# Performance work log

Measured on AMD Instinct MI355X. Metric: run time of the kernel, lower is better.

The kernel has to match this reference:

```python
import jax, jax.numpy as jnp
import numpy as np

B, N, J = 8, 2048, 1024
QD, CD, H, D = 1024, 768, 16, 64
INNER = H * D


def setup_inputs() -> dict:
    key = jax.random.key(0)
    ks = jax.random.split(key, 7)
    s = 0.02
    return {
        "x": jax.random.normal(ks[0], (B, N, QD), jnp.float32),
        "context": jax.random.normal(ks[1], (B, J, CD), jnp.float32),
        "Wq": jax.random.normal(ks[2], (QD, INNER), jnp.float32) * s,
        "Wk": jax.random.normal(ks[3], (CD, INNER), jnp.float32) * s,
        "Wv": jax.random.normal(ks[4], (CD, INNER), jnp.float32) * s,
        "Wo": jax.random.normal(ks[5], (INNER, QD), jnp.float32) * s,
        "bo": jnp.zeros((QD,), jnp.float32),
    }


def reference(x, context, Wq, Wk, Wv, Wo, bo):
    scale = D ** (-0.5)
    # projections, then split heads: b n (h d) -> b h n d
    q = (x @ Wq).reshape(B, N, H, D).transpose(0, 2, 1, 3)
    k = (context @ Wk).reshape(B, J, H, D).transpose(0, 2, 1, 3)
    v = (context @ Wv).reshape(B, J, H, D).transpose(0, 2, 1, 3)
    sim = jnp.einsum("bhid,bhjd->bhij", q, k) * scale  # [B,H,N,J]
    attn = jax.nn.softmax(sim, axis=-1)
    out = jnp.einsum("bhij,bhjd->bhid", attn, v)  # [B,H,N,D]
    out = out.transpose(0, 2, 1, 3).reshape(B, N, INNER)
    return out @ Wo + bo
```

## Files before the change

kernel.cpp:

```cpp
#include <hip/hip_runtime.h>

#define B_     8
#define N_     2048
#define J_     1024
#define QD_    1024
#define CD_    768
#define H_     16
#define D_     64
#define INNER_ 1024

typedef __attribute__((ext_vector_type(8)))  __bf16 bf16x8;
typedef __attribute__((ext_vector_type(4)))  __bf16 bf16x4;
typedef __attribute__((ext_vector_type(4)))  float  f32x4;
typedef __attribute__((ext_vector_type(16))) float  f32x16;
typedef __attribute__((ext_vector_type(2)))  unsigned uint2v;

__device__ __forceinline__ __bf16 to_bf16(float f) { return (__bf16)f; }

__device__ __forceinline__ unsigned pack2(float lo, float hi) {
    union { __bf16 h; unsigned short u; } a, b;
    a.h = (__bf16)lo; b.h = (__bf16)hi;
    return (unsigned)a.u | ((unsigned)b.u << 16);
}

__global__ __launch_bounds__(256)
void cvt_all(const float* __restrict__ x, const float* __restrict__ ctx,
             __bf16* __restrict__ xb, __bf16* __restrict__ cb)
{
    const int nx = (B_ * N_ * QD_) / 4;
    const int nc = (B_ * J_ * CD_) / 4;
    int i = blockIdx.x * 256 + threadIdx.x;
    if (i < nx) {
        float4 v = ((const float4*)x)[i];
        bf16x4 o;
        o[0] = (__bf16)v.x; o[1] = (__bf16)v.y; o[2] = (__bf16)v.z; o[3] = (__bf16)v.w;
        ((bf16x4*)xb)[i] = o;
    } else if (i < nx + nc) {
        float4 v = ((const float4*)ctx)[i - nx];
        bf16x4 o;
        o[0] = (__bf16)v.x; o[1] = (__bf16)v.y; o[2] = (__bf16)v.z; o[3] = (__bf16)v.w;
        ((bf16x4*)cb)[i - nx] = o;
    }
}

__global__ __launch_bounds__(256)
void transpose_all(const float* __restrict__ Wq, const float* __restrict__ Wk,
                   const float* __restrict__ Wv, const float* __restrict__ Wo,
                   __bf16* __restrict__ wqt, __bf16* __restrict__ wkt,
                   __bf16* __restrict__ wvt, __bf16* __restrict__ wot, float sq)
{
    __shared__ float tile[32][33];
    const int z = blockIdx.z;
    const float* W;  __bf16* Wt;  int K;  float scale = 1.f;
    if (z == 0)      { W = Wq; Wt = wqt; K = QD_;   scale = sq; }
    else if (z == 1) { W = Wk; Wt = wkt; K = CD_; }
    else if (z == 2) { W = Wv; Wt = wvt; K = CD_; }
    else             { W = Wo; Wt = wot; K = INNER_; }
    const int N = 1024;
    const int n0 = blockIdx.x * 32;
    const int k0 = blockIdx.y * 32;
    if (k0 >= K) return;
    const int tx = threadIdx.x & 31;
    const int ty = threadIdx.x >> 5;
#pragma unroll
    for (int r = 0; r < 32; r += 8)
        tile[ty + r][tx] = W[(size_t)(k0 + ty + r) * N + n0 + tx];
    __syncthreads();
#pragma unroll
    for (int r = 0; r < 32; r += 8)
        Wt[(size_t)(n0 + ty + r) * K + k0 + tx] = to_bf16(tile[tx][ty + r] * scale);
}

template<int FINAL, int KDIM>
__device__ __forceinline__
void core8(const __bf16* __restrict__ A, const __bf16* __restrict__ Bt,
           __bf16* __restrict__ Cb, __bf16* __restrict__ Cb2, float* __restrict__ Cf,
           const float* __restrict__ bias, int N, int work,
           __bf16 (&sA)[2][16384], __bf16 (&sB)[2][16384])
{
    constexpr int NIT = KDIM / 64;

    const int tid = threadIdx.x;
    const int wid = tid >> 6;
    const int l   = tid & 63;
    const int lo  = l & 15, hi = (l >> 4) & 3;

    const int gn = N >> 8;
    const int m0 = (work / gn) * 256;
    const int n0 = (work % gn) * 256;

    const int wm  = (wid >> 2) * 128, wn = (wid & 3) * 64;
    const int wmr = (wid >> 2) * 8,   bnr = (wid & 3) * 4;

    int rOff[2], cOff[2], dOff[2];
#pragma unroll
    for (int n = 0; n < 2; ++n) {
        const int s = n * 8 + wid;
        rOff[n] = (s >> 1) * 16 + (l >> 2);
        cOff[n] = (s & 1) * 32 + (((l & 3) * 8) ^ (((l >> 5) & 1) * 16));
        dOff[n] = n * 4096 + wid * 512;
    }

    const int inner = lo * 32 + ((hi * 8) ^ ((lo >> 3) * 16));

    f32x4 acc[8][4] = {};
    bf16x8 af[4][2], bfr[4][2];

#define STAGE8(nb, h, kt) do { \
    _Pragma("unroll") \
    for (int n = 0; n < 2; ++n) { \
        const __bf16* gp = ((h) < 2 ? A + (size_t)(m0 + ((h) & 1) * 128 + rOff[n]) * KDIM \
                                    : Bt + (size_t)(n0 + ((h) & 1) * 128 + rOff[n]) * KDIM) \
                           + (kt) + cOff[n]; \
        __bf16* dp = ((h) < 2 ? &sA[nb][((h) & 1) * 8192 + dOff[n]] \
                              : &sB[nb][((h) & 1) * 8192 + dOff[n]]); \
        __builtin_amdgcn_global_load_lds((const __attribute__((address_space(1))) void*)gp, \
                                         (__attribute__((address_space(3))) void*)dp, 16, 0, 0); \
    } } while (0)

#define RD_A(x0, cnt, nb) do { \
    _Pragma("unroll") \
    for (int x = 0; x < (cnt); ++x) \
        _Pragma("unroll") \
        for (int kk = 0; kk < 2; ++kk) \
            af[x][kk] = *(const bf16x8*)&sA[nb][((wmr + (x0) + x) * 2 + kk) * 512 + inner]; \
    } while (0)

#define RD_B(j0, cnt, nb) do { \
    _Pragma("unroll") \
    for (int j = 0; j < (cnt); ++j) \
        _Pragma("unroll") \
        for (int kk = 0; kk < 2; ++kk) \
            bfr[(j0) + j][kk] = *(const bf16x8*)&sB[nb][((bnr + (j0) + j) * 2 + kk) * 512 + inner]; \
    } while (0)

#define MMQ(mh, nh) do { \
    __builtin_amdgcn_s_setprio(1); \
    _Pragma("unroll") \
    for (int x = 0; x < 4; ++x) \
        _Pragma("unroll") \
        for (int j = 0; j < 2; ++j) \
            _Pragma("unroll") \
            for (int kk = 0; kk < 2; ++kk) \
                acc[(mh) * 4 + x][(nh) * 2 + j] = __builtin_amdgcn_mfma_f32_16x16x32_bf16( \
                    af[x][kk], bfr[(nh) * 2 + j][kk], acc[(mh) * 4 + x][(nh) * 2 + j], 0, 0, 0); \
    __builtin_amdgcn_s_setprio(0); \
    } while (0)

#define BARR() do { __builtin_amdgcn_s_barrier(); \
    asm volatile("" ::: "memory"); __builtin_amdgcn_sched_barrier(0); } while (0)

#pragma unroll
    for (int h = 0; h < 4; ++h) STAGE8(0, h, 0);

    for (int it = 0; it < NIT; ++it) {
        const int nb = it & 1, nbn = nb ^ 1;
        const int ktn = (it + 1) * 64;
        const bool notlast = (it < NIT - 1);

        if (notlast) STAGE8(nbn, 0, ktn);
        if (notlast) asm volatile("s_waitcnt vmcnt(2)" ::: "memory");
        else         asm volatile("s_waitcnt vmcnt(0)" ::: "memory");
        BARR();
        RD_A(0, 4, nb); RD_B(0, 2, nb);
        MMQ(0, 0);
        BARR();
        if (notlast) STAGE8(nbn, 1, ktn);
        BARR();
        RD_B(2, 2, nb);
        MMQ(0, 1);
        BARR();
        if (notlast) STAGE8(nbn, 2, ktn);
        BARR();
        RD_A(4, 4, nb);
        MMQ(1, 0);
        BARR();
        if (notlast) STAGE8(nbn, 3, ktn);
        BARR();
        MMQ(1, 1);
        BARR();
    }
#undef STAGE8
#undef RD_A
#undef RD_B
#undef MMQ
#undef BARR

#pragma unroll
    for (int i = 0; i < 8; ++i) {
        const int row = m0 + wm + i * 16 + hi * 4;
#pragma unroll
        for (int j = 0; j < 4; ++j) {
            const int col = n0 + wn + j * 16 + lo;
            if (FINAL == 3) {
                if (col < 1024) {
#pragma unroll
                    for (int r = 0; r < 4; ++r)
                        Cb[(size_t)(row + r) * 1024 + col] = to_bf16(acc[i][j][r]);
                } else {
                    const int c2 = col - 1024;
                    const int head = c2 >> 6, d = c2 & 63;
                    const int bb = row >> 10, jj = row & 1023;
                    bf16x4 v4;
#pragma unroll
                    for (int r = 0; r < 4; ++r) v4[r] = to_bf16(acc[i][j][r]);
                    *(bf16x4*)&Cb2[(((size_t)(bb * 16 + head)) * 64 + d) * (size_t)J_ + jj] = v4;
                }
            } else {
#pragma unroll
                for (int r = 0; r < 4; ++r) {
                    if (FINAL == 1) Cf[(size_t)(row + r) * N + col] = acc[i][j][r] + bias[col];
                    else            Cb[(size_t)(row + r) * N + col] = to_bf16(acc[i][j][r]);
                }
            }
        }
    }
}

__global__ __launch_bounds__(512, 2)
void gemm_qkv(const __bf16* __restrict__ xb, const __bf16* __restrict__ wqt, __bf16* __restrict__ Qb,
              const __bf16* __restrict__ cb, const __bf16* __restrict__ wkt,
              __bf16* __restrict__ Kb, __bf16* __restrict__ Vt)
{
    __shared__ __bf16 sA[2][16384];
    __shared__ __bf16 sB[2][16384];
    const int blk = blockIdx.x;
    if (blk < 256) {
        const int work = (blk & 7) * 32 + (blk >> 3);
        core8<0, QD_>(xb, wqt, Qb, nullptr, nullptr, nullptr, INNER_, work, sA, sB);
    } else {
        const int hb = blk - 256;
        const int work = (hb & 7) * 32 + (hb >> 3);
        core8<3, CD_>(cb, wkt, Kb, Vt, nullptr, nullptr, 2 * INNER_, work, sA, sB);
    }
}

__global__ __launch_bounds__(512, 2)
void gemm_o(const __bf16* __restrict__ Ob, const __bf16* __restrict__ wot,
            float* __restrict__ out, const float* __restrict__ bias)
{
    __shared__ __bf16 sA[2][16384];
    __shared__ __bf16 sB[2][16384];
    const int blk = blockIdx.x;
    const int work = (blk & 7) * 32 + (blk >> 3);
    core8<1, INNER_>(Ob, wot, nullptr, nullptr, out, bias, QD_, work, sA, sB);
}

#define SEGE 544

__global__ __launch_bounds__(256, 4)
void attn2(const __bf16* __restrict__ Qb, const __bf16* __restrict__ Kb,
           const __bf16* __restrict__ Vt, __bf16* __restrict__ Ob)
{
    __shared__ __bf16 sK[2][8 * SEGE];
    __shared__ __bf16 sV[2][8 * SEGE];

    const int tid = threadIdx.x;
    const int wid = tid >> 6;
    const int l   = tid & 63;
    const int lq  = l & 31;
    const int hi  = l >> 5;

    const int blk  = blockIdx.x;
    const int work = (blk & 7) * 256 + (blk >> 3);
    const int qt = work & 15;
    const int h  = (work >> 4) & 15;
    const int b  = work >> 8;
    const int bh = b * H_ + h;

    bf16x8 qf[4];
    {
        const __bf16* qp = Qb + ((size_t)b * N_ + qt * 128 + wid * 32 + lq) * INNER_ + h * D_;
#pragma unroll
        for (int kc = 0; kc < 4; ++kc)
            qf[kc] = *(const bf16x8*)(qp + kc * 16 + hi * 8);
    }

    f32x16 accO[2] = {};
    float lsum = 0.f;

    const int srow = l >> 3, schk = l & 7;
    const __bf16* ksrc = Kb + ((size_t)b * J_ + wid * 8 + srow) * INNER_ + h * D_ + ((schk ^ srow) * 8);
    const __bf16* vsrc = Vt + ((size_t)bh * D_ + wid * 8 + srow) * J_ + ((schk ^ srow) * 8);

#define STAGE_T(bb, t) do { \
    _Pragma("unroll") \
    for (int c = 0; c < 2; ++c) { \
        __builtin_amdgcn_global_load_lds((const __attribute__((address_space(1))) void*)(ksrc + ((size_t)(t) * 64 + c * 32) * INNER_), \
            (__attribute__((address_space(3))) void*)(&sK[bb][(c * 4 + wid) * SEGE]), 16, 0, 0); \
        __builtin_amdgcn_global_load_lds((const __attribute__((address_space(1))) void*)(vsrc + (size_t)(c) * 32 * J_ + (t) * 64), \
            (__attribute__((address_space(3))) void*)(&sV[bb][(c * 4 + wid) * SEGE]), 16, 0, 0); \
    } } while (0)

    STAGE_T(0, 0);
    __syncthreads();

    for (int t = 0; t < J_ / 64; ++t) {
        const int bb = t & 1;
        if (t < J_ / 64 - 1) STAGE_T(bb ^ 1, t + 1);

        const __bf16* Ks = sK[bb];
        const __bf16* Vs = sV[bb];

#pragma unroll
        for (int jsub = 0; jsub < 2; ++jsub) {
            bf16x8 kf[4], vf[2][2];
            const int ksg = (jsub * 4 + (lq >> 3)) * SEGE + (lq & 7) * 64;
#pragma unroll
            for (int kc = 0; kc < 4; ++kc)
                kf[kc] = *(const bf16x8*)&Ks[ksg + (((kc * 2 + hi) ^ (lq & 7)) * 8)];
#pragma unroll
            for (int dt = 0; dt < 2; ++dt) {
                const int vsg = (dt * 4 + (lq >> 3)) * SEGE + (lq & 7) * 64;
#pragma unroll
                for (int k2 = 0; k2 < 2; ++k2)
                    vf[dt][k2] = *(const bf16x8*)&Vs[vsg + ((((jsub * 2 + k2) * 2 + hi) ^ (lq & 7)) * 8)];
            }

            f32x16 s = {};
            __builtin_amdgcn_s_setprio(1);
#pragma unroll
            for (int kc = 0; kc < 4; ++kc)
                s = __builtin_amdgcn_mfma_f32_32x32x16_bf16(kf[kc], qf[kc], s, 0, 0, 0);
            __builtin_amdgcn_s_setprio(0);

            float p[16];
#pragma unroll
            for (int r = 0; r < 16; ++r)
                p[r] = __builtin_amdgcn_exp2f(s[r]);
            {
                float t0 = (p[0] + p[1]) + (p[2] + p[3]);
                float t1 = (p[4] + p[5]) + (p[6] + p[7]);
                float t2 = (p[8] + p[9]) + (p[10] + p[11]);
                float t3 = (p[12] + p[13]) + (p[14] + p[15]);
                lsum += (t0 + t1) + (t2 + t3);
            }

#pragma unroll
            for (int k2 = 0; k2 < 2; ++k2) {
                unsigned a0 = pack2(p[k2 * 8 + 0], p[k2 * 8 + 1]);
                unsigned a1 = pack2(p[k2 * 8 + 2], p[k2 * 8 + 3]);
                unsigned b0 = pack2(p[k2 * 8 + 4], p[k2 * 8 + 5]);
                unsigned b1 = pack2(p[k2 * 8 + 6], p[k2 * 8 + 7]);
                uint2v r0 = __builtin_amdgcn_permlane32_swap(a0, b0, false, false);
                uint2v r1 = __builtin_amdgcn_permlane32_swap(a1, b1, false, false);
                union { unsigned u[4]; bf16x8 v; } pu;
                pu.u[0] = r0[0];
                pu.u[1] = r1[0];
                pu.u[2] = r0[1];
                pu.u[3] = r1[1];
                __builtin_amdgcn_s_setprio(1);
#pragma unroll
                for (int dt = 0; dt < 2; ++dt)
                    accO[dt] = __builtin_amdgcn_mfma_f32_32x32x16_bf16(vf[dt][k2], pu.v, accO[dt], 0, 0, 0);
                __builtin_amdgcn_s_setprio(0);
            }
        }
        __syncthreads();
    }
#undef STAGE_T

    {
        float lt = lsum + __shfl_xor(lsum, 32);
        float inv = 1.f / lt;
        __bf16* op = Ob + ((size_t)b * N_ + qt * 128 + wid * 32 + lq) * INNER_ + h * D_;
#pragma unroll
        for (int dt = 0; dt < 2; ++dt)
#pragma unroll
            for (int g = 0; g < 4; ++g) {
                bf16x4 v4;
#pragma unroll
                for (int e = 0; e < 4; ++e) v4[e] = to_bf16(accO[dt][g * 4 + e] * inv);
                *(bf16x4*)&op[dt * 32 + g * 8 + hi * 4] = v4;
            }
    }
}

extern "C" void kernel_launch(void* const* d_in, const int* in_sizes, int n_in,
                              void* d_out, int out_size, void* d_ws, size_t ws_size,
                              hipStream_t stream)
{
    const float* x   = (const float*)d_in[0];
    const float* ctx = (const float*)d_in[1];
    const float* Wq  = (const float*)d_in[2];
    const float* Wk  = (const float*)d_in[3];
    const float* Wv  = (const float*)d_in[4];
    const float* Wo  = (const float*)d_in[5];
    const float* bo  = (const float*)d_in[6];
    float* out = (float*)d_out;

    char* w = (char*)d_ws;
    auto take = [&](size_t bytes) { char* p = w; w += bytes; return p; };
    __bf16* xb  = (__bf16*)take((size_t)B_ * N_ * QD_ * 2);
    __bf16* cb  = (__bf16*)take((size_t)B_ * J_ * CD_ * 2);
    __bf16* wqt = (__bf16*)take((size_t)QD_ * INNER_ * 2);
    __bf16* wkt = (__bf16*)take((size_t)CD_ * INNER_ * 2);
    __bf16* wvt = (__bf16*)take((size_t)CD_ * INNER_ * 2);
    __bf16* wot = (__bf16*)take((size_t)INNER_ * QD_ * 2);
    __bf16* Qb  = (__bf16*)take((size_t)B_ * N_ * INNER_ * 2);
    __bf16* Kb  = (__bf16*)take((size_t)B_ * J_ * INNER_ * 2);
    __bf16* Vt  = (__bf16*)take((size_t)B_ * J_ * INNER_ * 2);
    __bf16* Ob  = xb;

    const float SCALE_Q = 0.125f * 1.44269504088896f;

    const int ncvt = (B_ * N_ * QD_ + B_ * J_ * CD_) / 4;
    cvt_all<<<(ncvt + 255) / 256, 256, 0, stream>>>(x, ctx, xb, cb);
    transpose_all<<<dim3(32, 32, 4), 256, 0, stream>>>(Wq, Wk, Wv, Wo, wqt, wkt, wvt, wot, SCALE_Q);

    gemm_qkv<<<512, 512, 0, stream>>>(xb, wqt, Qb, cb, wkt, Kb, Vt);

    attn2<<<(N_ / 128) * H_ * B_, 256, 0, stream>>>(Qb, Kb, Vt, Ob);

    gemm_o<<<256, 512, 0, stream>>>(Ob, wot, out, bo);
}
```

Measured before the change: 244.9 us.

## Merge convert and transpose kernels; split PV accumulators to break MFMA dependency

Merges the bf16 input-conversion kernel and the weight-transpose kernel into one launch, with the block index picking which task a block does. This removes one kernel launch and the gap between the two. Separately, the attention kernel now keeps two independent output accumulators, one per k2 half, and sums them at the end. This breaks the serial dependency chain between back-to-back MFMAs at the cost of 32 more accumulator registers, which may reduce occupancy.

```diff
diff --git a/kernel.cpp b/kernel.cpp
--- a/kernel.cpp
+++ b/kernel.cpp
@@ -23,43 +23,46 @@
     return (unsigned)a.u | ((unsigned)b.u << 16);
 }
 
+#define NCVT_BLK 22528
+
 __global__ __launch_bounds__(256)
-void cvt_all(const float* __restrict__ x, const float* __restrict__ ctx,
-             __bf16* __restrict__ xb, __bf16* __restrict__ cb)
-{
-    const int nx = (B_ * N_ * QD_) / 4;
-    const int nc = (B_ * J_ * CD_) / 4;
-    int i = blockIdx.x * 256 + threadIdx.x;
-    if (i < nx) {
-        float4 v = ((const float4*)x)[i];
-        bf16x4 o;
-        o[0] = (__bf16)v.x; o[1] = (__bf16)v.y; o[2] = (__bf16)v.z; o[3] = (__bf16)v.w;
-        ((bf16x4*)xb)[i] = o;
-    } else if (i < nx + nc) {
-        float4 v = ((const float4*)ctx)[i - nx];
-        bf16x4 o;
-        o[0] = (__bf16)v.x; o[1] = (__bf16)v.y; o[2] = (__bf16)v.z; o[3] = (__bf16)v.w;
-        ((bf16x4*)cb)[i - nx] = o;
-    }
-}
-
-__global__ __launch_bounds__(256)
-void transpose_all(const float* __restrict__ Wq, const float* __restrict__ Wk,
-                   const float* __restrict__ Wv, const float* __restrict__ Wo,
-                   __bf16* __restrict__ wqt, __bf16* __restrict__ wkt,
-                   __bf16* __restrict__ wvt, __bf16* __restrict__ wot, float sq)
+void aux_all(const float* __restrict__ x, const float* __restrict__ ctx,
+             __bf16* __restrict__ xb, __bf16* __restrict__ cb,
+             const float* __restrict__ Wq, const float* __restrict__ Wk,
+             const float* __restrict__ Wv, const float* __restrict__ Wo,
+             __bf16* __restrict__ wqt, __bf16* __restrict__ wkt,
+             __bf16* __restrict__ wvt, __bf16* __restrict__ wot, float sq)
 {
     __shared__ float tile[32][33];
-    const int z = blockIdx.z;
+    const int blk = blockIdx.x;
+    if (blk < NCVT_BLK) {
+        const int nx = (B_ * N_ * QD_) / 4;
+        const int nc = (B_ * J_ * CD_) / 4;
+        int i = blk * 256 + threadIdx.x;
+        if (i < nx) {
+            float4 v = ((const float4*)x)[i];
+            bf16x4 o;
+            o[0] = (__bf16)v.x; o[1] = (__bf16)v.y; o[2] = (__bf16)v.z; o[3] = (__bf16)v.w;
+            ((bf16x4*)xb)[i] = o;
+        } else if (i < nx + nc) {
+            float4 v = ((const float4*)ctx)[i - nx];
+            bf16x4 o;
+            o[0] = (__bf16)v.x; o[1] = (__bf16)v.y; o[2] = (__bf16)v.z; o[3] = (__bf16)v.w;
+            ((bf16x4*)cb)[i - nx] = o;
+        }
+        return;
+    }
+    const int tb = blk - NCVT_BLK;
+    const int z  = tb >> 10;
+    const int k0 = ((tb >> 5) & 31) * 32;
+    const int n0 = (tb & 31) * 32;
     const float* W;  __bf16* Wt;  int K;  float scale = 1.f;
     if (z == 0)      { W = Wq; Wt = wqt; K = QD_;   scale = sq; }
     else if (z == 1) { W = Wk; Wt = wkt; K = CD_; }
     else if (z == 2) { W = Wv; Wt = wvt; K = CD_; }
     else             { W = Wo; Wt = wot; K = INNER_; }
+    if (k0 >= K) return;
     const int N = 1024;
-    const int n0 = blockIdx.x * 32;
-    const int k0 = blockIdx.y * 32;
-    if (k0 >= K) return;
     const int tx = threadIdx.x & 31;
     const int ty = threadIdx.x >> 5;
 #pragma unroll
@@ -276,7 +279,7 @@
             qf[kc] = *(const bf16x8*)(qp + kc * 16 + hi * 8);
     }
 
-    f32x16 accO[2] = {};
+    f32x16 accO[2][2] = {};
     float lsum = 0.f;
 
     const int srow = l >> 3, schk = l & 7;
@@ -352,7 +355,7 @@
                 __builtin_amdgcn_s_setprio(1);
 #pragma unroll
                 for (int dt = 0; dt < 2; ++dt)
-                    accO[dt] = __builtin_amdgcn_mfma_f32_32x32x16_bf16(vf[dt][k2], pu.v, accO[dt], 0, 0, 0);
+                    accO[k2][dt] = __builtin_amdgcn_mfma_f32_32x32x16_bf16(vf[dt][k2], pu.v, accO[k2][dt], 0, 0, 0);
                 __builtin_amdgcn_s_setprio(0);
             }
         }
@@ -365,14 +368,16 @@
         float inv = 1.f / lt;
         __bf16* op = Ob + ((size_t)b * N_ + qt * 128 + wid * 32 + lq) * INNER_ + h * D_;
 #pragma unroll
-        for (int dt = 0; dt < 2; ++dt)
+        for (int dt = 0; dt < 2; ++dt) {
+            f32x16 am = accO[0][dt] + accO[1][dt];
 #pragma unroll
             for (int g = 0; g < 4; ++g) {
                 bf16x4 v4;
 #pragma unroll
-                for (int e = 0; e < 4; ++e) v4[e] = to_bf16(accO[dt][g * 4 + e] * inv);
+                for (int e = 0; e < 4; ++e) v4[e] = to_bf16(am[g * 4 + e] * inv);
                 *(bf16x4*)&op[dt * 32 + g * 8 + hi * 4] = v4;
             }
+        }
     }
 }
 
@@ -404,9 +409,9 @@
 
     const float SCALE_Q = 0.125f * 1.44269504088896f;
 
-    const int ncvt = (B_ * N_ * QD_ + B_ * J_ * CD_) / 4;
-    cvt_all<<<(ncvt + 255) / 256, 256, 0, stream>>>(x, ctx, xb, cb);
-    transpose_all<<<dim3(32, 32, 4), 256, 0, stream>>>(Wq, Wk, Wv, Wo, wqt, wkt, wvt, wot, SCALE_Q);
+    aux_all<<<NCVT_BLK + 4096, 256, 0, stream>>>(x, ctx, xb, cb,
+                                                 Wq, Wk, Wv, Wo,
+                                                 wqt, wkt, wvt, wot, SCALE_Q);
 
     gemm_qkv<<<512, 512, 0, stream>>>(xb, wqt, Qb, cb, wkt, Kb, Vt);
 
```

Measured after the change: 608.6 us. 2.48x slower.
